# Optimization experiments

Measured on AMD Instinct MI355X. Metric: run time of the kernel, lower is better.

Reference implementation:

```python
import jax, jax.numpy as jnp
import numpy as np

DIM = 512
HID = 512
H = 8
HD = HID // H
RB_HID = 64
COORD = 3


def setup_inputs() -> dict:
    key = jax.random.key(0)
    ks = jax.random.split(key, 12)
    B, Nq, Nk = 2, 1024, 2048
    s = 0.02
    return {
        "q_in": jax.random.normal(ks[0], (B, Nq, DIM), jnp.float32),
        "kv_in": jax.random.normal(ks[1], (B, Nk, DIM), jnp.float32),
        "q_coords": jax.random.normal(ks[2], (B, Nq, COORD), jnp.float32),
        "kv_coords": jax.random.normal(ks[3], (B, Nk, COORD), jnp.float32),
        "Wq": jax.random.normal(ks[4], (DIM, HID), jnp.float32) * s,
        "Wk": jax.random.normal(ks[5], (DIM, HID), jnp.float32) * s,
        "Wv": jax.random.normal(ks[6], (DIM, HID), jnp.float32) * s,
        "Wo": jax.random.normal(ks[7], (HID, DIM), jnp.float32) * s,
        "W1": jax.random.normal(ks[8], (1, RB_HID), jnp.float32) * s,
        "b1": jnp.zeros((RB_HID,), jnp.float32),
        "W2": jax.random.normal(ks[9], (RB_HID, H), jnp.float32) * s,
        "b2": jnp.zeros((H,), jnp.float32),
    }


def reference(q_in, kv_in, q_coords, kv_coords, Wq, Wk, Wv, Wo, W1, b1, W2, b2):
    B, Nq, _ = q_in.shape
    Nk = kv_in.shape[1]
    # projections -> [B, H, N, HD]
    q = (q_in @ Wq).reshape(B, Nq, H, HD).transpose(0, 2, 1, 3)
    k = (kv_in @ Wk).reshape(B, Nk, H, HD).transpose(0, 2, 1, 3)
    v = (kv_in @ Wv).reshape(B, Nk, H, HD).transpose(0, 2, 1, 3)
    # pairwise Euclidean distance [B, Nq, Nk]
    diff = q_coords[:, :, None, :] - kv_coords[:, None, :, :]
    d = jnp.sqrt(jnp.sum(diff * diff, axis=-1))
    # 2-layer MLP on distance -> per-head bias [B, H, Nq, Nk]
    h = jax.nn.silu(d[..., None] * W1[0] + b1)  # [B,Nq,Nk,RB_HID]
    bias = (h @ W2 + b2).transpose(0, 3, 1, 2)  # [B,H,Nq,Nk]
    scale = HD ** -0.5
    logits = jnp.einsum("bhqd,bhkd->bhqk", q, k) * scale + bias
    attn = jax.nn.softmax(logits, axis=-1)
    out = jnp.einsum("bhqk,bhkd->bhqd", attn, v)
    out = out.transpose(0, 2, 1, 3).reshape(B, Nq, HID)
    return out @ Wo
```

## Files before the change

### kernel.cpp

```cpp
#include <hip/hip_runtime.h>
#include <hip/hip_bf16.h>
#include <math.h>

typedef short bf16x8 __attribute__((ext_vector_type(8)));
typedef float f32x4 __attribute__((ext_vector_type(4)));
typedef unsigned short u16;
typedef unsigned int u32;

#define NH 8
#define BB 2
#define NQ 1024
#define NK 2048
#define NSPLIT 8
#define M2CONST 6.4921250
#define SC2 0.18033688f
#define LS 68

#define MFMA16(a, b, c) __builtin_amdgcn_mfma_f32_16x16x32_bf16(a, b, c, 0, 0, 0)

__device__ __constant__ double XN_D[6] = {15.727406610312546, 13.656854249492380,
                                          10.070552360820166, 5.9294476391798335,
                                          2.3431457505076194, 0.27259338968745405};
#define XN0 15.727406610312546f
#define XN1 13.656854249492380f
#define XN2 10.070552360820166f
#define XN3 5.9294476391798335f
#define XN4 2.3431457505076194f

static __device__ __forceinline__ u32 bfr(float x) {
  u32 u = __builtin_bit_cast(u32, x);
  return u + 0x7FFFu + ((u >> 16) & 1u);
}
static __device__ __forceinline__ u32 pk2(float lo, float hi) {
  return (bfr(lo) >> 16) | (bfr(hi) & 0xFFFF0000u);
}
static __device__ __forceinline__ u16 bfs(float x) { return (u16)(bfr(x) >> 16); }

static __device__ __forceinline__ bf16x8 pack8(float4 a, float4 b) {
  union { bf16x8 v; uint4 u; } cv;
  cv.u.x = pk2(a.x, a.y);
  cv.u.y = pk2(a.z, a.w);
  cv.u.z = pk2(b.x, b.y);
  cv.u.w = pk2(b.z, b.w);
  return cv.v;
}

__global__ __launch_bounds__(256) void setup_kernel(
    const float* __restrict__ Wq, const float* __restrict__ Wk,
    const float* __restrict__ Wv, const float* __restrict__ Wo,
    u16* __restrict__ Tq, u16* __restrict__ Tk,
    u16* __restrict__ Tv, u16* __restrict__ To,
    const float* __restrict__ W1, const float* __restrict__ b1,
    const float* __restrict__ W2, const float* __restrict__ b2,
    float* __restrict__ polyc,
    const float* __restrict__ kc, u16* __restrict__ keg) {
  const int blk = blockIdx.x, t = threadIdx.x;
  if (blk < 256) {
    __shared__ u16 tile[64][65];
    const float* W; u16* Wt;
    switch (blk >> 6) {
      case 0: W = Wq; Wt = Tq; break;
      case 1: W = Wk; Wt = Tk; break;
      case 2: W = Wv; Wt = Tv; break;
      default: W = Wo; Wt = To; break;
    }
    const int rem = blk & 63;
    const int k0 = (rem >> 3) * 64, n0 = (rem & 7) * 64;
    const int r = t >> 4, c4 = (t & 15) * 4;
    #pragma unroll
    for (int p = 0; p < 4; p++) {
      int row = p * 16 + r;
      float4 v = *(const float4*)&W[(size_t)(k0 + row) * 512 + n0 + c4];
      tile[row][c4 + 0] = bfs(v.x);
      tile[row][c4 + 1] = bfs(v.y);
      tile[row][c4 + 2] = bfs(v.z);
      tile[row][c4 + 3] = bfs(v.w);
    }
    __syncthreads();
    #pragma unroll
    for (int p = 0; p < 4; p++) {
      int n = p * 16 + r;
      u16 u0 = tile[c4 + 0][n], u1 = tile[c4 + 1][n];
      u16 u2 = tile[c4 + 2][n], u3 = tile[c4 + 3][n];
      uint2 o;
      o.x = u0 | ((u32)u1 << 16);
      o.y = u2 | ((u32)u3 << 16);
      *(uint2*)&Wt[(size_t)(n0 + n) * 512 + k0 + c4] = o;
    }
  } else if (blk == 256) {
    __shared__ double fv[6][8];
    if (t < 48) {
      int i = t >> 3, h = t & 7;
      double x = XN_D[i];
      double acc = (double)b2[h];
      for (int r = 0; r < 64; r++) {
        double u = x * (double)W1[r] + (double)b1[r];
        double s = u / (1.0 + exp(-u));
        acc += s * (double)W2[r * 8 + h];
      }
      fv[i][h] = acc * 1.4426950408889634 - M2CONST;
    }
    __syncthreads();
    if (t < 8) {
      int h = t;
      double c[6];
      #pragma unroll
      for (int i = 0; i < 6; i++) c[i] = fv[i][h];
      for (int k = 1; k < 6; k++)
        for (int i = 5; i >= k; i--)
          c[i] = (c[i] - c[i - 1]) / (XN_D[i] - XN_D[i - k]);
      #pragma unroll
      for (int j = 0; j < 6; j++) polyc[h * 8 + j] = (float)c[j];
    }
  } else {
    int r = (blk - 257) * 256 + t;
    float kx = kc[(size_t)r * 3], ky = kc[(size_t)r * 3 + 1], kz = kc[(size_t)r * 3 + 2];
    uint4 o;
    o.x = pk2(-2.0f * kx, -2.0f * ky);
    o.y = pk2(-2.0f * kz, 1.0f);
    o.z = (u32)bfs(kx * kx + ky * ky + kz * kz);
    o.w = 0;
    *(uint4*)&keg[(size_t)r * 8] = o;
  }
}

__global__ __launch_bounds__(256) void gemm_qkv(
    const float* __restrict__ q_in, const float* __restrict__ kv_in,
    const u16* __restrict__ Wqt, const u16* __restrict__ Wkt,
    const u16* __restrict__ Wvt, u16* __restrict__ Qp,
    u16* __restrict__ Kp, u16* __restrict__ Vtp) {
  __shared__ u16 As[64 * LS];
  __shared__ u16 Bs[64 * LS];
  __shared__ u16 Bs2[64 * LS];
  const int t = threadIdx.x;
  const int w = t >> 6, l = t & 63, g = l >> 4, li = l & 15;
  const int bx = blockIdx.x;
  const bool isQ = bx < 32;
  const int m0 = (isQ ? bx : bx - 32) * 64, n0 = blockIdx.y * 64;
  const float* A = isQ ? q_in : kv_in;
  const u16* B1 = isQ ? Wqt : Wkt;
  const int ms = (w & 1) * 32, ns = (w >> 1) * 32;
  const int ar = t >> 2, ac = (t & 3) * 16;
  f32x4 acc[2][2] = {}, accV[2][2] = {};

  for (int kt = 0; kt < 512; kt += 64) {
    float4 a4[4];
    #pragma unroll
    for (int q = 0; q < 4; q++)
      a4[q] = *(const float4*)&A[(size_t)(m0 + ar) * 512 + kt + ac + 4 * q];
    bf16x8 bk[2], bv2[2];
    #pragma unroll
    for (int p = 0; p < 2; p++) {
      int f = p * 256 + t, r = f >> 3, c8 = (f & 7) * 8;
      bk[p] = *(const bf16x8*)&B1[(size_t)(n0 + r) * 512 + kt + c8];
    }
    if (!isQ) {
      #pragma unroll
      for (int p = 0; p < 2; p++) {
        int f = p * 256 + t, r = f >> 3, c8 = (f & 7) * 8;
        bv2[p] = *(const bf16x8*)&Wvt[(size_t)(n0 + r) * 512 + kt + c8];
      }
    }
    __syncthreads();
    *(bf16x8*)&As[ar * LS + ac] = pack8(a4[0], a4[1]);
    *(bf16x8*)&As[ar * LS + ac + 8] = pack8(a4[2], a4[3]);
    #pragma unroll
    for (int p = 0; p < 2; p++) {
      int f = p * 256 + t, r = f >> 3, c8 = (f & 7) * 8;
      *(bf16x8*)&Bs[r * LS + c8] = bk[p];
    }
    if (!isQ) {
      #pragma unroll
      for (int p = 0; p < 2; p++) {
        int f = p * 256 + t, r = f >> 3, c8 = (f & 7) * 8;
        *(bf16x8*)&Bs2[r * LS + c8] = bv2[p];
      }
    }
    __syncthreads();
    #pragma unroll
    for (int ks = 0; ks < 2; ks++) {
      bf16x8 a0 = *(const bf16x8*)&As[(ms + li) * LS + ks * 32 + g * 8];
      bf16x8 a1 = *(const bf16x8*)&As[(ms + 16 + li) * LS + ks * 32 + g * 8];
      bf16x8 k0 = *(const bf16x8*)&Bs[(ns + li) * LS + ks * 32 + g * 8];
      bf16x8 k1 = *(const bf16x8*)&Bs[(ns + 16 + li) * LS + ks * 32 + g * 8];
      acc[0][0] = MFMA16(a0, k0, acc[0][0]);
      acc[0][1] = MFMA16(a0, k1, acc[0][1]);
      acc[1][0] = MFMA16(a1, k0, acc[1][0]);
      acc[1][1] = MFMA16(a1, k1, acc[1][1]);
      if (!isQ) {
        bf16x8 v0 = *(const bf16x8*)&Bs2[(ns + li) * LS + ks * 32 + g * 8];
        bf16x8 v1 = *(const bf16x8*)&Bs2[(ns + 16 + li) * LS + ks * 32 + g * 8];
        accV[0][0] = MFMA16(a0, v0, accV[0][0]);
        accV[0][1] = MFMA16(a0, v1, accV[0][1]);
        accV[1][0] = MFMA16(a1, v0, accV[1][0]);
        accV[1][1] = MFMA16(a1, v1, accV[1][1]);
      }
    }
  }
  #pragma unroll
  for (int mi = 0; mi < 2; mi++) {
    #pragma unroll
    for (int ni = 0; ni < 2; ni++) {
      int row = m0 + ms + mi * 16 + 4 * g;
      int col = n0 + ns + ni * 16 + li;
      f32x4 vk = acc[mi][ni];
      if (isQ) {
        #pragma unroll
        for (int r = 0; r < 4; r++) Qp[(size_t)(row + r) * 512 + col] = bfs(vk[r]);
      } else {
        #pragma unroll
        for (int r = 0; r < 4; r++) Kp[(size_t)(row + r) * 512 + col] = bfs(vk[r]);
        f32x4 vv = accV[mi][ni];
        int bb = row >> 11, j = row & 2047;
        int hh = col >> 6, d = col & 63;
        uint2 o;
        o.x = pk2(vv[0], vv[1]);
        o.y = pk2(vv[2], vv[3]);
        *(uint2*)&Vtp[((size_t)((bb * 8 + hh) * 64 + d)) * 2048 + j] = o;
      }
    }
  }
}

__global__ __launch_bounds__(256, 6) void attn_kernel(
    const u16* __restrict__ Qb, const u16* __restrict__ Kb,
    const u16* __restrict__ Vt, const float* __restrict__ qc,
    const u16* __restrict__ keg, const float* __restrict__ polyc,
    float* __restrict__ Op, float* __restrict__ Lp) {
  __shared__ u16 Kl[64 * LS];
  __shared__ u16 Vtl[64 * LS];
  __shared__ u16 Pl[64 * LS];

  const int t = threadIdx.x;
  const int w = t >> 6, l = t & 63, g = l >> 4, li = l & 15;
  const int qt = blockIdx.x >> 3, sidx = blockIdx.x & 7;
  const int h = blockIdx.y, b = blockIdx.z;

  const float c0 = polyc[h * 8 + 0], c1 = polyc[h * 8 + 1];
  const float c2 = polyc[h * 8 + 2], c3 = polyc[h * 8 + 3];
  const float c4 = polyc[h * 8 + 4], c5 = polyc[h * 8 + 5];

  const int qrow = qt * 64 + w * 16 + li;
  const size_t qg = (size_t)b * NQ + qrow;
  bf16x8 qf0 = *(const bf16x8*)&Qb[qg * 512 + h * 64 + g * 8];
  bf16x8 qf1 = *(const bf16x8*)&Qb[qg * 512 + h * 64 + 32 + g * 8];
  float qx = qc[qg * 3], qy = qc[qg * 3 + 1], qz = qc[qg * 3 + 2];
  bf16x8 qe = {};
  if (g == 0) {
    qe[0] = (short)bfs(qx);
    qe[1] = (short)bfs(qy);
    qe[2] = (short)bfs(qz);
    qe[3] = (short)bfs(qx * qx + qy * qy + qz * qz);
    qe[4] = (short)bfs(1.0f);
  }

  f32x4 oacc[4] = {};
  float lacc = 0.0f;

  const u16* Kg = Kb + (size_t)b * NK * 512 + h * 64;
  const u16* Vg = Vt + (size_t)((b * 8 + h) * 64) * 2048;
  const u16* keg_b = keg + (size_t)b * NK * 8;

  for (int it = 0; it < NK / NSPLIT / 64; it++) {
    const int jbase = sidx * (NK / NSPLIT) + it * 64;
    __syncthreads();
    #pragma unroll
    for (int pp = 0; pp < 2; pp++) {
      int f = pp * 256 + t, row = f >> 3, c8 = (f & 7) * 8;
      *(bf16x8*)&Kl[row * LS + c8] =
          *(const bf16x8*)&Kg[(size_t)(jbase + row) * 512 + c8];
      *(bf16x8*)&Vtl[row * LS + c8] =
          *(const bf16x8*)&Vg[(size_t)row * 2048 + jbase + c8];
    }
    __syncthreads();

    f32x4 sac[4], dac[4];
    #pragma unroll
    for (int j4 = 0; j4 < 4; j4++) {
      bf16x8 ka0 = *(const bf16x8*)&Kl[(j4 * 16 + li) * LS + g * 8];
      bf16x8 ka1 = *(const bf16x8*)&Kl[(j4 * 16 + li) * LS + 32 + g * 8];
      f32x4 z = {};
      f32x4 s0 = MFMA16(ka0, qf0, z);
      sac[j4] = MFMA16(ka1, qf1, s0);
      bf16x8 ke = {};
      if (g == 0)
        ke = *(const bf16x8*)&keg_b[(size_t)(jbase + j4 * 16 + li) * 8];
      dac[j4] = MFMA16(ke, qe, z);
    }

    #pragma unroll
    for (int j4 = 0; j4 < 4; j4++) {
      float p[4];
      #pragma unroll
      for (int r = 0; r < 4; r++) {
        float u = fmaxf(dac[j4][r], 0.0f);
        float d = fminf(__builtin_amdgcn_sqrtf(u), 16.0f);
        float gp = c5;
        gp = fmaf(gp, d - XN4, c4);
        gp = fmaf(gp, d - XN3, c3);
        gp = fmaf(gp, d - XN2, c2);
        gp = fmaf(gp, d - XN1, c1);
        gp = fmaf(gp, d - XN0, c0);
        p[r] = __builtin_amdgcn_exp2f(fmaf(sac[j4][r], SC2, gp));
        lacc += p[r];
      }
      uint2 pv;
      pv.x = pk2(p[0], p[1]);
      pv.y = pk2(p[2], p[3]);
      *(uint2*)&Pl[(w * 16 + li) * LS + j4 * 16 + g * 4] = pv;
    }

    bf16x8 pf0 = *(const bf16x8*)&Pl[(w * 16 + li) * LS + g * 8];
    bf16x8 pf1 = *(const bf16x8*)&Pl[(w * 16 + li) * LS + 32 + g * 8];
    #pragma unroll
    for (int dt = 0; dt < 4; dt++) {
      bf16x8 v0 = *(const bf16x8*)&Vtl[(dt * 16 + li) * LS + g * 8];
      bf16x8 v1 = *(const bf16x8*)&Vtl[(dt * 16 + li) * LS + 32 + g * 8];
      oacc[dt] = MFMA16(pf0, v0, oacc[dt]);
      oacc[dt] = MFMA16(pf1, v1, oacc[dt]);
    }
  }

  float lf = lacc;
  lf += __shfl_xor(lf, 16);
  lf += __shfl_xor(lf, 32);

  const size_t obase =
      ((size_t)(sidx * 16 + b * 8 + h) * 1024 + qt * 64 + w * 16) * 64;
  #pragma unroll
  for (int dt = 0; dt < 4; dt++)
    #pragma unroll
    for (int r = 0; r < 4; r++)
      Op[obase + (size_t)(4 * g + r) * 64 + dt * 16 + li] = oacc[dt][r];
  if (g == 0)
    Lp[(size_t)(sidx * 16 + b * 8 + h) * 1024 + qt * 64 + w * 16 + li] = lf;
}

__global__ __launch_bounds__(256) void combine_kernel(const float* __restrict__ Op,
                                                      const float* __restrict__ Lp,
                                                      u16* __restrict__ AOb) {
  int tid = blockIdx.x * 256 + threadIdx.x;
  int d4 = tid & 15, rh = tid >> 4;
  int bh = rh >> 10, qrow = rh & 1023;
  f32x4 o = {};
  float lsum = 0.0f;
  #pragma unroll
  for (int s = 0; s < NSPLIT; s++) {
    f32x4 v = *(const f32x4*)&Op[((size_t)(s * 16 + bh) * 1024 + qrow) * 64 + d4 * 4];
    o += v;
    lsum += Lp[(size_t)(s * 16 + bh) * 1024 + qrow];
  }
  float inv = __builtin_amdgcn_rcpf(lsum);
  uint2 pk;
  pk.x = pk2(o[0] * inv, o[1] * inv);
  pk.y = pk2(o[2] * inv, o[3] * inv);
  *(uint2*)&AOb[((size_t)(bh >> 3) * NQ + qrow) * 512 + (bh & 7) * 64 + d4 * 4] = pk;
}

__global__ __launch_bounds__(256) void gemm_wo(const u16* __restrict__ A,
                                               const u16* __restrict__ Bt,
                                               float* __restrict__ C) {
  __shared__ u16 As[32 * LS];
  __shared__ u16 Bs[64 * LS];
  const int t = threadIdx.x;
  const int w = t >> 6, l = t & 63, g = l >> 4, li = l & 15;
  const int m0 = blockIdx.x * 32, n0 = blockIdx.y * 64;
  const int ms = (w & 1) * 16, ns = (w >> 1) * 32;
  f32x4 acc[2] = {};
  for (int kt = 0; kt < 512; kt += 64) {
    bf16x8 av, bv[2];
    {
      int r = t >> 3, c8 = (t & 7) * 8;
      av = *(const bf16x8*)&A[(size_t)(m0 + r) * 512 + kt + c8];
    }
    #pragma unroll
    for (int p = 0; p < 2; p++) {
      int f = p * 256 + t, r = f >> 3, c8 = (f & 7) * 8;
      bv[p] = *(const bf16x8*)&Bt[(size_t)(n0 + r) * 512 + kt + c8];
    }
    __syncthreads();
    {
      int r = t >> 3, c8 = (t & 7) * 8;
      *(bf16x8*)&As[r * LS + c8] = av;
    }
    #pragma unroll
    for (int p = 0; p < 2; p++) {
      int f = p * 256 + t, r = f >> 3, c8 = (f & 7) * 8;
      *(bf16x8*)&Bs[r * LS + c8] = bv[p];
    }
    __syncthreads();
    #pragma unroll
    for (int ks = 0; ks < 2; ks++) {
      bf16x8 af = *(const bf16x8*)&As[(ms + li) * LS + ks * 32 + g * 8];
      bf16x8 b0 = *(const bf16x8*)&Bs[(ns + li) * LS + ks * 32 + g * 8];
      bf16x8 b1 = *(const bf16x8*)&Bs[(ns + 16 + li) * LS + ks * 32 + g * 8];
      acc[0] = MFMA16(af, b0, acc[0]);
      acc[1] = MFMA16(af, b1, acc[1]);
    }
  }
  #pragma unroll
  for (int ni = 0; ni < 2; ni++) {
    f32x4 v = acc[ni];
    int row = m0 + ms + 4 * g;
    int col = n0 + ns + ni * 16 + li;
    #pragma unroll
    for (int r = 0; r < 4; r++) C[(size_t)(row + r) * 512 + col] = v[r];
  }
}

extern "C" void kernel_launch(void* const* d_in, const int* in_sizes, int n_in,
                              void* d_out, int out_size, void* d_ws, size_t ws_size,
                              hipStream_t stream) {
  const float* q_in      = (const float*)d_in[0];
  const float* kv_in     = (const float*)d_in[1];
  const float* q_coords  = (const float*)d_in[2];
  const float* kv_coords = (const float*)d_in[3];
  const float* Wq        = (const float*)d_in[4];
  const float* Wk        = (const float*)d_in[5];
  const float* Wv        = (const float*)d_in[6];
  const float* Wo        = (const float*)d_in[7];
  const float* W1        = (const float*)d_in[8];
  const float* b1        = (const float*)d_in[9];
  const float* W2        = (const float*)d_in[10];
  const float* b2        = (const float*)d_in[11];

  char* p = (char*)d_ws;
  u16* Wqt  = (u16*)p; p += (size_t)512 * 512 * 2;
  u16* Wkt  = (u16*)p; p += (size_t)512 * 512 * 2;
  u16* Wvt  = (u16*)p; p += (size_t)512 * 512 * 2;
  u16* Wot  = (u16*)p; p += (size_t)512 * 512 * 2;
  u16* Qp   = (u16*)p; p += (size_t)2048 * 512 * 2;
  u16* Kp   = (u16*)p; p += (size_t)4096 * 512 * 2;
  u16* Vtp  = (u16*)p; p += (size_t)4096 * 512 * 2;
  u16* AOb  = (u16*)p; p += (size_t)2048 * 512 * 2;
  u16* keg  = (u16*)p; p += (size_t)4096 * 8 * 2;
  float* polyc = (float*)p; p += (size_t)64 * 4;
  p = (char*)(((size_t)p + 255) & ~(size_t)255);
  float* Opart = (float*)p; p += (size_t)NSPLIT * 16 * 1024 * 64 * 4;
  float* Lpart = (float*)p; p += (size_t)NSPLIT * 16 * 1024 * 4;

  setup_kernel<<<273, 256, 0, stream>>>(Wq, Wk, Wv, Wo, Wqt, Wkt, Wvt, Wot,
                                        W1, b1, W2, b2, polyc, kv_coords, keg);
  gemm_qkv<<<dim3(96, 8), 256, 0, stream>>>(q_in, kv_in, Wqt, Wkt, Wvt,
                                            Qp, Kp, Vtp);
  attn_kernel<<<dim3(128, 8, 2), 256, 0, stream>>>(Qp, Kp, Vtp, q_coords, keg,
                                                   polyc, Opart, Lpart);
  combine_kernel<<<1024, 256, 0, stream>>>(Opart, Lpart, AOb);
  gemm_wo<<<dim3(64, 8), 256, 0, stream>>>(AOb, Wot, (float*)d_out);
}
```

Measured before the change: 153.2 us.

## Fit bias polynomial in squared distance and prefetch K/V tiles into registers

The distance-bias polynomial is now interpolated over squared distance and converted to monomial form. This removes the per-element sqrt and the node subtractions from the softmax inner loop, but the clamp changes (the lower clamp at zero is gone) and fitting in d² may lose accuracy. K and V tiles for the next iteration are loaded into registers while the current tile is being computed, overlapping global loads with MFMA work. The score and exp loops are fused and the occupancy hint drops from 6 to 4 waves to leave room for the extra registers.

```diff
diff --git a/kernel.cpp b/kernel.cpp
--- a/kernel.cpp
+++ b/kernel.cpp
@@ -18,14 +18,9 @@
 
 #define MFMA16(a, b, c) __builtin_amdgcn_mfma_f32_16x16x32_bf16(a, b, c, 0, 0, 0)
 
-__device__ __constant__ double XN_D[6] = {15.727406610312546, 13.656854249492380,
-                                          10.070552360820166, 5.9294476391798335,
-                                          2.3431457505076194, 0.27259338968745405};
-#define XN0 15.727406610312546f
-#define XN1 13.656854249492380f
-#define XN2 10.070552360820166f
-#define XN3 5.9294476391798335f
-#define XN4 2.3431457505076194f
+__device__ __constant__ double XN_D[6] = {251.63850576500074, 218.50966799187810,
+                                          161.12883777312265, 94.871162226877350,
+                                          37.490330081221910, 4.3614942349992570};
 
 static __device__ __forceinline__ u32 bfr(float x) {
   u32 u = __builtin_bit_cast(u32, x);
@@ -91,7 +86,7 @@
     __shared__ double fv[6][8];
     if (t < 48) {
       int i = t >> 3, h = t & 7;
-      double x = XN_D[i];
+      double x = sqrt(XN_D[i]);
       double acc = (double)b2[h];
       for (int r = 0; r < 64; r++) {
         double u = x * (double)W1[r] + (double)b1[r];
@@ -109,8 +104,18 @@
       for (int k = 1; k < 6; k++)
         for (int i = 5; i >= k; i--)
           c[i] = (c[i] - c[i - 1]) / (XN_D[i] - XN_D[i - k]);
+      double m[6] = {c[5], 0, 0, 0, 0, 0};
+      int deg = 0;
+      for (int i = 4; i >= 0; i--) {
+        double np[6] = {};
+        for (int j = deg; j >= 0; j--) np[j + 1] += m[j];
+        for (int j = 0; j <= deg; j++) np[j] -= XN_D[i] * m[j];
+        np[0] += c[i];
+        deg++;
+        for (int j = 0; j <= deg; j++) m[j] = np[j];
+      }
       #pragma unroll
-      for (int j = 0; j < 6; j++) polyc[h * 8 + j] = (float)c[j];
+      for (int j = 0; j < 6; j++) polyc[h * 8 + j] = (float)m[j];
     }
   } else {
     int r = (blk - 257) * 256 + t;
@@ -222,7 +227,7 @@
   }
 }
 
-__global__ __launch_bounds__(256, 6) void attn_kernel(
+__global__ __launch_bounds__(256, 4) void attn_kernel(
     const u16* __restrict__ Qb, const u16* __restrict__ Kb,
     const u16* __restrict__ Vt, const float* __restrict__ qc,
     const u16* __restrict__ keg, const float* __restrict__ polyc,
@@ -261,49 +266,50 @@
   const u16* Vg = Vt + (size_t)((b * 8 + h) * 64) * 2048;
   const u16* keg_b = keg + (size_t)b * NK * 8;
 
+  const int jb0 = sidx * (NK / NSPLIT);
+  const int srow = t >> 3, sc8 = (t & 7) * 8;
+
+  bf16x8 kr0 = *(const bf16x8*)&Kg[(size_t)(jb0 + srow) * 512 + sc8];
+  bf16x8 kr1 = *(const bf16x8*)&Kg[(size_t)(jb0 + 32 + srow) * 512 + sc8];
+  bf16x8 vr0 = *(const bf16x8*)&Vg[(size_t)srow * 2048 + jb0 + sc8];
+  bf16x8 vr1 = *(const bf16x8*)&Vg[(size_t)(32 + srow) * 2048 + jb0 + sc8];
+
   for (int it = 0; it < NK / NSPLIT / 64; it++) {
-    const int jbase = sidx * (NK / NSPLIT) + it * 64;
-    __syncthreads();
-    #pragma unroll
-    for (int pp = 0; pp < 2; pp++) {
-      int f = pp * 256 + t, row = f >> 3, c8 = (f & 7) * 8;
-      *(bf16x8*)&Kl[row * LS + c8] =
-          *(const bf16x8*)&Kg[(size_t)(jbase + row) * 512 + c8];
-      *(bf16x8*)&Vtl[row * LS + c8] =
-          *(const bf16x8*)&Vg[(size_t)row * 2048 + jbase + c8];
-    }
-    __syncthreads();
-
-    f32x4 sac[4], dac[4];
+    const int jbase = jb0 + it * 64;
+    __syncthreads();
+    *(bf16x8*)&Kl[srow * LS + sc8] = kr0;
+    *(bf16x8*)&Kl[(32 + srow) * LS + sc8] = kr1;
+    *(bf16x8*)&Vtl[srow * LS + sc8] = vr0;
+    *(bf16x8*)&Vtl[(32 + srow) * LS + sc8] = vr1;
+    __syncthreads();
+    if (it + 1 < NK / NSPLIT / 64) {
+      const int jn = jbase + 64;
+      kr0 = *(const bf16x8*)&Kg[(size_t)(jn + srow) * 512 + sc8];
+      kr1 = *(const bf16x8*)&Kg[(size_t)(jn + 32 + srow) * 512 + sc8];
+      vr0 = *(const bf16x8*)&Vg[(size_t)srow * 2048 + jn + sc8];
+      vr1 = *(const bf16x8*)&Vg[(size_t)(32 + srow) * 2048 + jn + sc8];
+    }
+
     #pragma unroll
     for (int j4 = 0; j4 < 4; j4++) {
       bf16x8 ka0 = *(const bf16x8*)&Kl[(j4 * 16 + li) * LS + g * 8];
       bf16x8 ka1 = *(const bf16x8*)&Kl[(j4 * 16 + li) * LS + 32 + g * 8];
       f32x4 z = {};
       f32x4 s0 = MFMA16(ka0, qf0, z);
-      sac[j4] = MFMA16(ka1, qf1, s0);
+      f32x4 sac = MFMA16(ka1, qf1, s0);
       bf16x8 ke = {};
       if (g == 0)
         ke = *(const bf16x8*)&keg_b[(size_t)(jbase + j4 * 16 + li) * 8];
-      dac[j4] = MFMA16(ke, qe, z);
-    }
-
-    #pragma unroll
-    for (int j4 = 0; j4 < 4; j4++) {
+      f32x4 dac = MFMA16(ke, qe, z);
+
       float p[4];
       #pragma unroll
       for (int r = 0; r < 4; r++) {
-        float u = fmaxf(dac[j4][r], 0.0f);
-        float d = fminf(__builtin_amdgcn_sqrtf(u), 16.0f);
-        float gp = c5;
-        gp = fmaf(gp, d - XN4, c4);
-        gp = fmaf(gp, d - XN3, c3);
-        gp = fmaf(gp, d - XN2, c2);
-        gp = fmaf(gp, d - XN1, c1);
-        gp = fmaf(gp, d - XN0, c0);
-        p[r] = __builtin_amdgcn_exp2f(fmaf(sac[j4][r], SC2, gp));
-        lacc += p[r];
-      }
+        float u = fminf(dac[r], 256.0f);
+        float gp = fmaf(fmaf(fmaf(fmaf(fmaf(c5, u, c4), u, c3), u, c2), u, c1), u, c0);
+        p[r] = __builtin_amdgcn_exp2f(fmaf(sac[r], SC2, gp));
+      }
+      lacc += (p[0] + p[1]) + (p[2] + p[3]);
       uint2 pv;
       pv.x = pk2(p[0], p[1]);
       pv.y = pk2(p[2], p[3]);
```

After: 147.5 us. -3.7%, faster.
